# Kernel tuning notes

Measured on AMD Instinct MI355X. Metric: run time of the kernel, lower is better.

## Reference

```python
import jax, jax.numpy as jnp
import numpy as np
import math

D_MODEL = 128
N_HEADS = 4
DIM_FF = 256
B, L = 4, 2048
EPS = 1e-5
NEG = -1e9


def _layernorm(x, g, b):
    mu = jnp.mean(x, axis=-1, keepdims=True)
    var = jnp.mean((x - mu) ** 2, axis=-1, keepdims=True)
    return (x - mu) * jax.lax.rsqrt(var + EPS) * g + b


def setup_inputs() -> dict:
    key = jax.random.key(0)
    ks = jax.random.split(key, 16)
    s = 1.0 / math.sqrt(D_MODEL)
    return {
        "h": jax.random.normal(ks[0], (B, L, D_MODEL), jnp.float32),
        "attn_bias": jax.random.normal(ks[1], (B, N_HEADS, L, L), jnp.float32),
        "node_mask": jax.random.randint(ks[2], (B, L), 0, 2).astype(jnp.float32),
        "sparse_mask": jax.random.randint(ks[3], (B, L, L), 0, 2).astype(bool),
        "w_qkv": jax.random.normal(ks[4], (3 * D_MODEL, D_MODEL), jnp.float32) * s,
        "b_qkv": jnp.zeros((3 * D_MODEL,), jnp.float32),
        "w_out": jax.random.normal(ks[5], (D_MODEL, D_MODEL), jnp.float32) * s,
        "b_out": jnp.zeros((D_MODEL,), jnp.float32),
        "w_ff1": jax.random.normal(ks[6], (DIM_FF, D_MODEL), jnp.float32) * s,
        "b_ff1": jnp.zeros((DIM_FF,), jnp.float32),
        "w_ff2": jax.random.normal(ks[7], (D_MODEL, DIM_FF), jnp.float32) * (1.0 / math.sqrt(DIM_FF)),
        "b_ff2": jnp.zeros((D_MODEL,), jnp.float32),
        "ln1_g": jnp.ones((D_MODEL,), jnp.float32),
        "ln1_b": jnp.zeros((D_MODEL,), jnp.float32),
        "ln2_g": jnp.ones((D_MODEL,), jnp.float32),
        "ln2_b": jnp.zeros((D_MODEL,), jnp.float32),
    }


def reference(h, attn_bias, node_mask, sparse_mask, w_qkv, b_qkv, w_out, b_out,
              w_ff1, b_ff1, w_ff2, b_ff2, ln1_g, ln1_b, ln2_g, ln2_b):
    bsz, lsz, dsz = h.shape
    dk = dsz // N_HEADS
    qkv = h @ w_qkv.T + b_qkv  # [B,L,3D]
    q, k, v = jnp.split(qkv, 3, axis=-1)
    # [B,L,D] -> [B,H,L,dk]
    q = q.reshape(bsz, lsz, N_HEADS, dk).transpose(0, 2, 1, 3)
    k = k.reshape(bsz, lsz, N_HEADS, dk).transpose(0, 2, 1, 3)
    v = v.reshape(bsz, lsz, N_HEADS, dk).transpose(0, 2, 1, 3)
    scores = jnp.einsum("bhqd,bhkd->bhqk", q, k) / math.sqrt(dk)
    scores = scores + attn_bias
    scores = jnp.where(sparse_mask[:, None, :, :], scores, NEG)
    key_mask = node_mask[:, None, None, :] > 0
    scores = jnp.where(key_mask, scores, NEG)
    attn = jax.nn.softmax(scores, axis=-1)
    attn = attn * (node_mask[:, None, :, None] > 0).astype(attn.dtype)
    out = jnp.einsum("bhqk,bhkd->bhqd", attn, v)
    out = out.transpose(0, 2, 1, 3).reshape(bsz, lsz, dsz)
    out = out @ w_out.T + b_out
    h1 = _layernorm(h + out, ln1_g, ln1_b)
    ff = jax.nn.relu(h1 @ w_ff1.T + b_ff1) @ w_ff2.T + b_ff2
    h2 = _layernorm(h1 + ff, ln2_g, ln2_b)
    return h2 * node_mask[:, :, None]
```

## Files before the change

kernel.cpp:

```cpp
#include <hip/hip_runtime.h>
#include <math.h>

#define NEG_INF (-1e9f)
#define EPS 1e-5f

typedef __attribute__((ext_vector_type(8))) short short8;
typedef __attribute__((ext_vector_type(4))) float floatx4;

__device__ __forceinline__ unsigned short f2bf(float x) {
    union { float f; unsigned u; } v; v.f = x;
    unsigned r = v.u + 0x7fffu + ((v.u >> 16) & 1u);
    return (unsigned short)(r >> 16);
}

__global__ void detect_mask_kernel(const unsigned int* __restrict__ sm, int* __restrict__ flag) {
    __shared__ int bad;
    if (threadIdx.x == 0) bad = 0;
    __syncthreads();
    for (int i = threadIdx.x; i < 4096; i += 256) {
        if (sm[i] > 1u) bad = 1;
    }
    __syncthreads();
    if (threadIdx.x == 0) *flag = bad;
}

__global__ void nmask_pack_kernel(const float* __restrict__ nm, unsigned int* __restrict__ nmb) {
    const int t = threadIdx.x;
    const int b = t >> 6, w32 = t & 63;
    unsigned u = 0;
#pragma unroll
    for (int j = 0; j < 32; ++j)
        u |= (nm[b * 2048 + w32 * 32 + j] > 0.f ? 1u : 0u) << j;
    nmb[t] = u;
}

__global__ void mask_prep_kernel(const unsigned char* __restrict__ smraw,
                                 const int* __restrict__ flag,
                                 const unsigned int* __restrict__ nmb,
                                 unsigned int* __restrict__ cbits) {
    const int idx = blockIdx.x * 256 + threadIdx.x;
    const int b = idx >> 17;
    const int q = (idx >> 6) & 2047;
    const int w32 = idx & 63;
    unsigned u = 0;
    if (*flag) {
        const uint4* p = reinterpret_cast<const uint4*>(
            smraw + (size_t)(b * 2048 + q) * 2048 + w32 * 32);
        uint4 a = p[0], c = p[1];
        unsigned wd0 = a.x, wd1 = a.y, wd2 = a.z, wd3 = a.w;
        unsigned wd4 = c.x, wd5 = c.y, wd6 = c.z, wd7 = c.w;
#define BYTES4(v, sh) \
        u |= ((v) & 0xffu ? 1u : 0u) << (sh); \
        u |= ((v) & 0xff00u ? 1u : 0u) << ((sh) + 1); \
        u |= ((v) & 0xff0000u ? 1u : 0u) << ((sh) + 2); \
        u |= ((v) & 0xff000000u ? 1u : 0u) << ((sh) + 3);
        BYTES4(wd0, 0) BYTES4(wd1, 4) BYTES4(wd2, 8) BYTES4(wd3, 12)
        BYTES4(wd4, 16) BYTES4(wd5, 20) BYTES4(wd6, 24) BYTES4(wd7, 28)
#undef BYTES4
    } else {
        const uint4* p = reinterpret_cast<const uint4*>(
            reinterpret_cast<const unsigned int*>(smraw) + (size_t)(b * 2048 + q) * 2048 + w32 * 32);
#pragma unroll
        for (int wi = 0; wi < 8; ++wi) {
            uint4 a = p[wi];
            u |= (a.x ? 1u : 0u) << (wi * 4);
            u |= (a.y ? 1u : 0u) << (wi * 4 + 1);
            u |= (a.z ? 1u : 0u) << (wi * 4 + 2);
            u |= (a.w ? 1u : 0u) << (wi * 4 + 3);
        }
    }
    cbits[idx] = u & nmb[b * 64 + w32];
}

__global__ void transpose_kernel(const float* __restrict__ src, float* __restrict__ dst,
                                 int R, int C) {
    int idx = blockIdx.x * 256 + threadIdx.x;
    if (idx < R * C) {
        int r = idx / C, c = idx % C;
        dst[c * R + r] = src[idx];
    }
}

__global__ void qkv_kernel(const float* __restrict__ h, const float* __restrict__ wT,
                           const float* __restrict__ bqkv,
                           unsigned short* __restrict__ qb, unsigned short* __restrict__ kbm,
                           unsigned short* __restrict__ vtb) {
    __shared__ __align__(16) float hs[16 * 128];
    const int tid = threadIdx.x;
    const int row0 = blockIdx.x * 16;
    for (int i = tid; i < 2048; i += 384) hs[i] = h[row0 * 128 + i];
    __syncthreads();

    const int c = tid;
    float acc[16];
#pragma unroll
    for (int r = 0; r < 16; ++r) acc[r] = 0.f;

    for (int d0 = 0; d0 < 128; d0 += 4) {
        float w0 = wT[(d0 + 0) * 384 + c];
        float w1 = wT[(d0 + 1) * 384 + c];
        float w2 = wT[(d0 + 2) * 384 + c];
        float w3 = wT[(d0 + 3) * 384 + c];
#pragma unroll
        for (int r = 0; r < 16; ++r) {
            float4 h4 = *reinterpret_cast<const float4*>(&hs[r * 128 + d0]);
            acc[r] = fmaf(w0, h4.x, acc[r]);
            acc[r] = fmaf(w1, h4.y, acc[r]);
            acc[r] = fmaf(w2, h4.z, acc[r]);
            acc[r] = fmaf(w3, h4.w, acc[r]);
        }
    }
    const int part = c >> 7;
    const int cc = c & 127;
    const int head = cc >> 5;
    const int dd = cc & 31;
    const float bias = bqkv[c];
    const float scale = (part == 0) ? 0.17677669529663687f : 1.0f;
#pragma unroll
    for (int r = 0; r < 16; ++r) {
        int grow = row0 + r;
        int b = grow >> 11, l = grow & 2047;
        int bh = b * 4 + head;
        unsigned short val = f2bf((acc[r] + bias) * scale);
        if (part == 0)      qb[((size_t)bh * 2048 + l) * 32 + dd] = val;
        else if (part == 1) kbm[((size_t)bh * 2048 + l) * 32 + dd] = val;
        else                vtb[((size_t)bh * 32 + dd) * 2048 + l] = val;
    }
}

__global__ __launch_bounds__(256, 2) void attn_kernel(
        const unsigned short* __restrict__ qb, const unsigned short* __restrict__ kbm,
        const unsigned short* __restrict__ vtb, const float* __restrict__ bias,
        const unsigned int* __restrict__ cbits, const float* __restrict__ nmask,
        float* __restrict__ aout) {
    __shared__ unsigned short p_lds[4][16 * 72];

    const int tid = threadIdx.x;
    const int w = tid >> 6, L = tid & 63;
    const int lb = (blockIdx.x & 7) * 64 + (blockIdx.x >> 3);
    const int bh = lb >> 5, qt = lb & 31;
    const int b = bh >> 2, hh = bh & 3;
    const int q0 = qt * 64 + w * 16;
    const int q = L & 15, g = L >> 4;

    const unsigned short* kbase = kbm + (size_t)bh * 2048 * 32 + g * 8;
    const unsigned short* vbase = vtb + (size_t)bh * 32 * 2048 + g * 8;
    const short8 qf = *reinterpret_cast<const short8*>(
        qb + ((size_t)bh * 2048 + q0 + q) * 32 + g * 8);
    const float* brow = bias + ((size_t)bh * 2048 + q0 + q) * 2048 + g * 4;
    const unsigned int* crow = cbits + (size_t)(b * 2048 + q0 + q) * 64;

    float mrun = -3.0e38f, lrun = 0.f;
    floatx4 o0 = {0.f, 0.f, 0.f, 0.f}, o1 = {0.f, 0.f, 0.f, 0.f};
    const floatx4 zacc = {0.f, 0.f, 0.f, 0.f};
    unsigned short* pl = &p_lds[w][q * 72];

    for (int t = 0; t < 32; ++t) {
        const int k0 = t * 64;
        short8 kf0 = *reinterpret_cast<const short8*>(kbase + (size_t)(k0 +  0 + q) * 32);
        short8 kf1 = *reinterpret_cast<const short8*>(kbase + (size_t)(k0 + 16 + q) * 32);
        short8 kf2 = *reinterpret_cast<const short8*>(kbase + (size_t)(k0 + 32 + q) * 32);
        short8 kf3 = *reinterpret_cast<const short8*>(kbase + (size_t)(k0 + 48 + q) * 32);
        float4 bq0 = *reinterpret_cast<const float4*>(brow + k0);
        float4 bq1 = *reinterpret_cast<const float4*>(brow + k0 + 16);
        float4 bq2 = *reinterpret_cast<const float4*>(brow + k0 + 32);
        float4 bq3 = *reinterpret_cast<const float4*>(brow + k0 + 48);
        uint2 cw = *reinterpret_cast<const uint2*>(crow + t * 2);
        short8 vf00 = *reinterpret_cast<const short8*>(vbase + (size_t)(q     ) * 2048 + k0);
        short8 vf01 = *reinterpret_cast<const short8*>(vbase + (size_t)(q     ) * 2048 + k0 + 32);
        short8 vf10 = *reinterpret_cast<const short8*>(vbase + (size_t)(16 + q) * 2048 + k0);
        short8 vf11 = *reinterpret_cast<const short8*>(vbase + (size_t)(16 + q) * 2048 + k0 + 32);

        float s[16];
        {
            floatx4 r0 = __builtin_amdgcn_mfma_f32_16x16x32_bf16(kf0, qf, zacc, 0, 0, 0);
            floatx4 r1 = __builtin_amdgcn_mfma_f32_16x16x32_bf16(kf1, qf, zacc, 0, 0, 0);
            floatx4 r2 = __builtin_amdgcn_mfma_f32_16x16x32_bf16(kf2, qf, zacc, 0, 0, 0);
            floatx4 r3 = __builtin_amdgcn_mfma_f32_16x16x32_bf16(kf3, qf, zacc, 0, 0, 0);
            s[0] = r0[0]; s[1] = r0[1]; s[2] = r0[2]; s[3] = r0[3];
            s[4] = r1[0]; s[5] = r1[1]; s[6] = r1[2]; s[7] = r1[3];
            s[8] = r2[0]; s[9] = r2[1]; s[10] = r2[2]; s[11] = r2[3];
            s[12] = r3[0]; s[13] = r3[1]; s[14] = r3[2]; s[15] = r3[3];
        }
        float bvv[16];
        bvv[0] = bq0.x; bvv[1] = bq0.y; bvv[2] = bq0.z; bvv[3] = bq0.w;
        bvv[4] = bq1.x; bvv[5] = bq1.y; bvv[6] = bq1.z; bvv[7] = bq1.w;
        bvv[8] = bq2.x; bvv[9] = bq2.y; bvv[10] = bq2.z; bvv[11] = bq2.w;
        bvv[12] = bq3.x; bvv[13] = bq3.y; bvv[14] = bq3.z; bvv[15] = bq3.w;
#pragma unroll
        for (int i = 0; i < 16; ++i) {
            const int mm = i >> 2, reg = i & 3;
            const unsigned word = (mm < 2) ? cw.x : cw.y;
            const int sh = 16 * (mm & 1) + 4 * g + reg;
            const bool keep = (word >> sh) & 1;
            s[i] = keep ? (s[i] + bvv[i]) : NEG_INF;
        }
        float tm = s[0];
#pragma unroll
        for (int i = 1; i < 16; ++i) tm = fmaxf(tm, s[i]);
        tm = fmaxf(tm, __shfl_xor(tm, 16));
        tm = fmaxf(tm, __shfl_xor(tm, 32));
        const float mn = fmaxf(mrun, tm);
        const float f = __expf(mrun - mn);
        mrun = mn;
        float p[16], ts = 0.f;
#pragma unroll
        for (int i = 0; i < 16; ++i) { p[i] = __expf(s[i] - mn); ts += p[i]; }
        ts += __shfl_xor(ts, 16);
        ts += __shfl_xor(ts, 32);
        lrun = lrun * f + ts;
        o0 *= f; o1 *= f;
#pragma unroll
        for (int mm = 0; mm < 4; ++mm) {
            unsigned u0 = (unsigned)f2bf(p[4 * mm]) | ((unsigned)f2bf(p[4 * mm + 1]) << 16);
            unsigned u1 = (unsigned)f2bf(p[4 * mm + 2]) | ((unsigned)f2bf(p[4 * mm + 3]) << 16);
            *reinterpret_cast<unsigned int*>(pl + 16 * mm + 4 * g) = u0;
            *reinterpret_cast<unsigned int*>(pl + 16 * mm + 4 * g + 2) = u1;
        }
        short8 pb0 = *reinterpret_cast<const short8*>(pl + g * 8);
        short8 pb1 = *reinterpret_cast<const short8*>(pl + 32 + g * 8);
        o0 = __builtin_amdgcn_mfma_f32_16x16x32_bf16(vf00, pb0, o0, 0, 0, 0);
        o0 = __builtin_amdgcn_mfma_f32_16x16x32_bf16(vf01, pb1, o0, 0, 0, 0);
        o1 = __builtin_amdgcn_mfma_f32_16x16x32_bf16(vf10, pb0, o1, 0, 0, 0);
        o1 = __builtin_amdgcn_mfma_f32_16x16x32_bf16(vf11, pb1, o1, 0, 0, 0);
    }

    const int qrow = q0 + q;
    const float nmq = nmask[b * 2048 + qrow];
    const float inv = (nmq > 0.f) ? (1.f / lrun) : 0.f;
    float* op = aout + ((size_t)b * 2048 + qrow) * 128 + hh * 32 + g * 4;
    *reinterpret_cast<float4*>(op) = make_float4(o0[0] * inv, o0[1] * inv, o0[2] * inv, o0[3] * inv);
    *reinterpret_cast<float4*>(op + 16) = make_float4(o1[0] * inv, o1[1] * inv, o1[2] * inv, o1[3] * inv);
}

__device__ __forceinline__ void ln_stats(const float* buf, float* mu_s, float* rs_s, int tid) {
    int row = tid >> 4, sl = tid & 15;
    float4 x0 = *reinterpret_cast<const float4*>(&buf[row * 128 + sl * 8]);
    float4 x1 = *reinterpret_cast<const float4*>(&buf[row * 128 + sl * 8 + 4]);
    float sum = x0.x + x0.y + x0.z + x0.w + x1.x + x1.y + x1.z + x1.w;
    float sq = x0.x * x0.x + x0.y * x0.y + x0.z * x0.z + x0.w * x0.w +
               x1.x * x1.x + x1.y * x1.y + x1.z * x1.z + x1.w * x1.w;
#pragma unroll
    for (int off = 8; off > 0; off >>= 1) {
        sum += __shfl_xor(sum, off);
        sq += __shfl_xor(sq, off);
    }
    if (sl == 0) {
        float mu = sum * (1.f / 128.f);
        float var = sq * (1.f / 128.f) - mu * mu;
        mu_s[row] = mu;
        rs_s[row] = rsqrtf(var + EPS);
    }
}

__global__ void epilogue_kernel(const float* __restrict__ aout, const float* __restrict__ h,
                                const float* __restrict__ woutT, const float* __restrict__ bout,
                                const float* __restrict__ wff1T, const float* __restrict__ bff1,
                                const float* __restrict__ wff2T, const float* __restrict__ bff2,
                                const float* __restrict__ g1, const float* __restrict__ b1,
                                const float* __restrict__ g2, const float* __restrict__ b2,
                                const float* __restrict__ nmask, float* __restrict__ out) {
    __shared__ __align__(16) float A[16 * 128];
    __shared__ __align__(16) float Hb[16 * 128];
    __shared__ __align__(16) float F[16 * 256];
    __shared__ float mu_s[16], rs_s[16];

    const int tid = threadIdx.x;
    const int row0 = blockIdx.x * 16;
    for (int i = tid; i < 2048; i += 256) {
        A[i] = aout[row0 * 128 + i];
        Hb[i] = h[row0 * 128 + i];
    }
    __syncthreads();

    const int g = tid >> 7, c = tid & 127;

    float acc[8];
#pragma unroll
    for (int r = 0; r < 8; ++r) acc[r] = 0.f;
    for (int d0 = 0; d0 < 128; d0 += 4) {
        float w0 = woutT[(d0 + 0) * 128 + c];
        float w1 = woutT[(d0 + 1) * 128 + c];
        float w2 = woutT[(d0 + 2) * 128 + c];
        float w3 = woutT[(d0 + 3) * 128 + c];
#pragma unroll
        for (int r = 0; r < 8; ++r) {
            float4 a4 = *reinterpret_cast<const float4*>(&A[(g * 8 + r) * 128 + d0]);
            acc[r] = fmaf(w0, a4.x, acc[r]);
            acc[r] = fmaf(w1, a4.y, acc[r]);
            acc[r] = fmaf(w2, a4.z, acc[r]);
            acc[r] = fmaf(w3, a4.w, acc[r]);
        }
    }
    float bo = bout[c];
#pragma unroll
    for (int r = 0; r < 8; ++r) {
        int row = g * 8 + r;
        Hb[row * 128 + c] += acc[r] + bo;
    }
    __syncthreads();

    ln_stats(Hb, mu_s, rs_s, tid);
    __syncthreads();
    float g1c = g1[c], b1c = b1[c];
#pragma unroll
    for (int r = 0; r < 8; ++r) {
        int row = g * 8 + r;
        float v = (Hb[row * 128 + c] - mu_s[row]) * rs_s[row] * g1c + b1c;
        Hb[row * 128 + c] = v;
    }
    __syncthreads();

    {
        const int j = tid;
        float a2[16];
#pragma unroll
        for (int r = 0; r < 16; ++r) a2[r] = 0.f;
        for (int d0 = 0; d0 < 128; d0 += 4) {
            float w0 = wff1T[(d0 + 0) * 256 + j];
            float w1 = wff1T[(d0 + 1) * 256 + j];
            float w2 = wff1T[(d0 + 2) * 256 + j];
            float w3 = wff1T[(d0 + 3) * 256 + j];
#pragma unroll
            for (int r = 0; r < 16; ++r) {
                float4 h4 = *reinterpret_cast<const float4*>(&Hb[r * 128 + d0]);
                a2[r] = fmaf(w0, h4.x, a2[r]);
                a2[r] = fmaf(w1, h4.y, a2[r]);
                a2[r] = fmaf(w2, h4.z, a2[r]);
                a2[r] = fmaf(w3, h4.w, a2[r]);
            }
        }
        float bj = bff1[j];
#pragma unroll
        for (int r = 0; r < 16; ++r) F[r * 256 + j] = fmaxf(a2[r] + bj, 0.f);
    }
    __syncthreads();

    float a3[8];
#pragma unroll
    for (int r = 0; r < 8; ++r) a3[r] = 0.f;
    for (int d0 = 0; d0 < 256; d0 += 4) {
        float w0 = wff2T[(d0 + 0) * 128 + c];
        float w1 = wff2T[(d0 + 1) * 128 + c];
        float w2 = wff2T[(d0 + 2) * 128 + c];
        float w3 = wff2T[(d0 + 3) * 128 + c];
#pragma unroll
        for (int r = 0; r < 8; ++r) {
            float4 f4 = *reinterpret_cast<const float4*>(&F[(g * 8 + r) * 256 + d0]);
            a3[r] = fmaf(w0, f4.x, a3[r]);
            a3[r] = fmaf(w1, f4.y, a3[r]);
            a3[r] = fmaf(w2, f4.z, a3[r]);
            a3[r] = fmaf(w3, f4.w, a3[r]);
        }
    }
    float bo2 = bff2[c];
#pragma unroll
    for (int r = 0; r < 8; ++r) {
        int row = g * 8 + r;
        A[row * 128 + c] = a3[r] + bo2 + Hb[row * 128 + c];
    }
    __syncthreads();

    ln_stats(A, mu_s, rs_s, tid);
    __syncthreads();
    float g2c = g2[c], b2c = b2[c];
#pragma unroll
    for (int r = 0; r < 8; ++r) {
        int row = g * 8 + r;
        float nm = nmask[row0 + row];
        float v = (A[row * 128 + c] - mu_s[row]) * rs_s[row] * g2c + b2c;
        out[(row0 + row) * 128 + c] = v * nm;
    }
}

extern "C" void kernel_launch(void* const* d_in, const int* in_sizes, int n_in,
                              void* d_out, int out_size, void* d_ws, size_t ws_size,
                              hipStream_t stream) {
    const float* h = (const float*)d_in[0];
    const float* bias = (const float*)d_in[1];
    const float* nmask = (const float*)d_in[2];
    const void* smask = d_in[3];
    const float* w_qkv = (const float*)d_in[4];
    const float* b_qkv = (const float*)d_in[5];
    const float* w_out = (const float*)d_in[6];
    const float* b_out = (const float*)d_in[7];
    const float* w_ff1 = (const float*)d_in[8];
    const float* b_ff1 = (const float*)d_in[9];
    const float* w_ff2 = (const float*)d_in[10];
    const float* b_ff2 = (const float*)d_in[11];
    const float* g1 = (const float*)d_in[12];
    const float* b1 = (const float*)d_in[13];
    const float* g2 = (const float*)d_in[14];
    const float* b2 = (const float*)d_in[15];
    float* out = (float*)d_out;

    char* wsb = (char*)d_ws;
    float* aoutw = (float*)wsb;
    unsigned short* qb  = (unsigned short*)(wsb + (4 << 20));
    unsigned short* kbm = (unsigned short*)(wsb + (6 << 20));
    unsigned short* vtb = (unsigned short*)(wsb + (8 << 20));
    unsigned int* cbits = (unsigned int*)(wsb + (10 << 20));
    unsigned int* nmb   = (unsigned int*)(wsb + (12 << 20));
    float* wqkvT = (float*)(wsb + (12 << 20) + 4096);
    float* woutT = wqkvT + 384 * 128;
    float* wff1T = woutT + 128 * 128;
    float* wff2T = wff1T + 256 * 128;
    int* smflag = (int*)(wff2T + 128 * 256);

    detect_mask_kernel<<<1, 256, 0, stream>>>((const unsigned int*)smask, smflag);
    nmask_pack_kernel<<<1, 256, 0, stream>>>(nmask, nmb);
    mask_prep_kernel<<<2048, 256, 0, stream>>>((const unsigned char*)smask, smflag, nmb, cbits);
    transpose_kernel<<<192, 256, 0, stream>>>(w_qkv, wqkvT, 384, 128);
    transpose_kernel<<<64, 256, 0, stream>>>(w_out, woutT, 128, 128);
    transpose_kernel<<<128, 256, 0, stream>>>(w_ff1, wff1T, 256, 128);
    transpose_kernel<<<128, 256, 0, stream>>>(w_ff2, wff2T, 128, 256);
    qkv_kernel<<<512, 384, 0, stream>>>(h, wqkvT, b_qkv, qb, kbm, vtb);
    attn_kernel<<<512, 256, 0, stream>>>(qb, kbm, vtb, bias, cbits, nmask, aoutw);
    epilogue_kernel<<<512, 256, 0, stream>>>(aoutw, h, woutT, b_out, wff1T, b_ff1,
                                             wff2T, b_ff2, g1, b1, g2, b2, nmask, out);
}
```

Before: 191.2 us.

## Stage attention bias through LDS with register prefetch and merge tiny launches

The attention kernel now loads each 16x64 bias tile with row-coalesced float4 reads into registers, one tile ahead, then writes it to a padded LDS buffer and reads it back in the MFMA fragment layout. Before, each lane read scattered 16-byte pieces of global memory. The change targets the bias stream, the largest input at about 268 MB of fp32, by improving its coalescing and hiding its latency. It also merges the two mask-prep kernels into one launch and the four weight transposes into one, cutting launch overhead. The cost is more LDS and registers per block, which may lower occupancy. There is no barrier between the LDS write and read, so correctness relies on each wave using only its own LDS slice.

```diff
diff --git a/kernel.cpp b/kernel.cpp
--- a/kernel.cpp
+++ b/kernel.cpp
@@ -13,25 +13,26 @@
     return (unsigned short)(r >> 16);
 }
 
-__global__ void detect_mask_kernel(const unsigned int* __restrict__ sm, int* __restrict__ flag) {
-    __shared__ int bad;
-    if (threadIdx.x == 0) bad = 0;
-    __syncthreads();
-    for (int i = threadIdx.x; i < 4096; i += 256) {
-        if (sm[i] > 1u) bad = 1;
-    }
-    __syncthreads();
-    if (threadIdx.x == 0) *flag = bad;
-}
-
-__global__ void nmask_pack_kernel(const float* __restrict__ nm, unsigned int* __restrict__ nmb) {
-    const int t = threadIdx.x;
-    const int b = t >> 6, w32 = t & 63;
-    unsigned u = 0;
-#pragma unroll
-    for (int j = 0; j < 32; ++j)
-        u |= (nm[b * 2048 + w32 * 32 + j] > 0.f ? 1u : 0u) << j;
-    nmb[t] = u;
+__global__ void prep_kernel(const unsigned int* __restrict__ sm, int* __restrict__ flag,
+                            const float* __restrict__ nm, unsigned int* __restrict__ nmb) {
+    if (blockIdx.x == 0) {
+        __shared__ int bad;
+        if (threadIdx.x == 0) bad = 0;
+        __syncthreads();
+        for (int i = threadIdx.x; i < 4096; i += 256) {
+            if (sm[i] > 1u) bad = 1;
+        }
+        __syncthreads();
+        if (threadIdx.x == 0) *flag = bad;
+    } else {
+        const int t = threadIdx.x;
+        const int b = t >> 6, w32 = t & 63;
+        unsigned u = 0;
+#pragma unroll
+        for (int j = 0; j < 32; ++j)
+            u |= (nm[b * 2048 + w32 * 32 + j] > 0.f ? 1u : 0u) << j;
+        nmb[t] = u;
+    }
 }
 
 __global__ void mask_prep_kernel(const unsigned char* __restrict__ smraw,
@@ -72,12 +73,23 @@
     cbits[idx] = u & nmb[b * 64 + w32];
 }
 
-__global__ void transpose_kernel(const float* __restrict__ src, float* __restrict__ dst,
-                                 int R, int C) {
+__global__ void transpose_all_kernel(const float* __restrict__ w_qkv, const float* __restrict__ w_out,
+                                     const float* __restrict__ w_ff1, const float* __restrict__ w_ff2,
+                                     float* __restrict__ wqkvT, float* __restrict__ woutT,
+                                     float* __restrict__ wff1T, float* __restrict__ wff2T) {
     int idx = blockIdx.x * 256 + threadIdx.x;
-    if (idx < R * C) {
-        int r = idx / C, c = idx % C;
-        dst[c * R + r] = src[idx];
+    if (idx < 49152) {
+        int r = idx / 128, c = idx % 128;
+        wqkvT[c * 384 + r] = w_qkv[idx];
+    } else if (idx < 65536) {
+        int i = idx - 49152; int r = i / 128, c = i % 128;
+        woutT[c * 128 + r] = w_out[i];
+    } else if (idx < 98304) {
+        int i = idx - 65536; int r = i / 128, c = i % 128;
+        wff1T[c * 256 + r] = w_ff1[i];
+    } else {
+        int i = idx - 98304; int r = i / 256, c = i % 256;
+        wff2T[c * 128 + r] = w_ff2[i];
     }
 }
 
@@ -133,6 +145,7 @@
         const unsigned short* __restrict__ vtb, const float* __restrict__ bias,
         const unsigned int* __restrict__ cbits, const float* __restrict__ nmask,
         float* __restrict__ aout) {
+    __shared__ float bias_lds[4][16 * 68];
     __shared__ unsigned short p_lds[4][16 * 72];
 
     const int tid = threadIdx.x;
@@ -147,24 +160,39 @@
     const unsigned short* vbase = vtb + (size_t)bh * 32 * 2048 + g * 8;
     const short8 qf = *reinterpret_cast<const short8*>(
         qb + ((size_t)bh * 2048 + q0 + q) * 32 + g * 8);
-    const float* brow = bias + ((size_t)bh * 2048 + q0 + q) * 2048 + g * 4;
     const unsigned int* crow = cbits + (size_t)(b * 2048 + q0 + q) * 64;
+
+    const float* bias_wave = bias + ((size_t)bh * 2048 + q0) * 2048;
+    const int brow_ld = L >> 4;
+    const int bcol_ld = (L & 15) * 4;
+    float* blds = bias_lds[w];
 
     float mrun = -3.0e38f, lrun = 0.f;
     floatx4 o0 = {0.f, 0.f, 0.f, 0.f}, o1 = {0.f, 0.f, 0.f, 0.f};
     const floatx4 zacc = {0.f, 0.f, 0.f, 0.f};
     unsigned short* pl = &p_lds[w][q * 72];
 
+    float4 bpre[4];
+#pragma unroll
+    for (int i = 0; i < 4; ++i)
+        bpre[i] = *reinterpret_cast<const float4*>(
+            bias_wave + (size_t)(brow_ld + 4 * i) * 2048 + bcol_ld);
+
     for (int t = 0; t < 32; ++t) {
         const int k0 = t * 64;
+#pragma unroll
+        for (int i = 0; i < 4; ++i)
+            *reinterpret_cast<float4*>(blds + (brow_ld + 4 * i) * 68 + bcol_ld) = bpre[i];
+        const int k0n = (t + 1 < 32) ? k0 + 64 : 0;
+#pragma unroll
+        for (int i = 0; i < 4; ++i)
+            bpre[i] = *reinterpret_cast<const float4*>(
+                bias_wave + (size_t)(brow_ld + 4 * i) * 2048 + k0n + bcol_ld);
+
         short8 kf0 = *reinterpret_cast<const short8*>(kbase + (size_t)(k0 +  0 + q) * 32);
         short8 kf1 = *reinterpret_cast<const short8*>(kbase + (size_t)(k0 + 16 + q) * 32);
         short8 kf2 = *reinterpret_cast<const short8*>(kbase + (size_t)(k0 + 32 + q) * 32);
         short8 kf3 = *reinterpret_cast<const short8*>(kbase + (size_t)(k0 + 48 + q) * 32);
-        float4 bq0 = *reinterpret_cast<const float4*>(brow + k0);
-        float4 bq1 = *reinterpret_cast<const float4*>(brow + k0 + 16);
-        float4 bq2 = *reinterpret_cast<const float4*>(brow + k0 + 32);
-        float4 bq3 = *reinterpret_cast<const float4*>(brow + k0 + 48);
         uint2 cw = *reinterpret_cast<const uint2*>(crow + t * 2);
         short8 vf00 = *reinterpret_cast<const short8*>(vbase + (size_t)(q     ) * 2048 + k0);
         short8 vf01 = *reinterpret_cast<const short8*>(vbase + (size_t)(q     ) * 2048 + k0 + 32);
@@ -182,6 +210,10 @@
             s[8] = r2[0]; s[9] = r2[1]; s[10] = r2[2]; s[11] = r2[3];
             s[12] = r3[0]; s[13] = r3[1]; s[14] = r3[2]; s[15] = r3[3];
         }
+        float4 bq0 = *reinterpret_cast<const float4*>(blds + q * 68 +  0 + 4 * g);
+        float4 bq1 = *reinterpret_cast<const float4*>(blds + q * 68 + 16 + 4 * g);
+        float4 bq2 = *reinterpret_cast<const float4*>(blds + q * 68 + 32 + 4 * g);
+        float4 bq3 = *reinterpret_cast<const float4*>(blds + q * 68 + 48 + 4 * g);
         float bvv[16];
         bvv[0] = bq0.x; bvv[1] = bq0.y; bvv[2] = bq0.z; bvv[3] = bq0.w;
         bvv[4] = bq1.x; bvv[5] = bq1.y; bvv[6] = bq1.z; bvv[7] = bq1.w;
@@ -407,13 +439,10 @@
     float* wff2T = wff1T + 256 * 128;
     int* smflag = (int*)(wff2T + 128 * 256);
 
-    detect_mask_kernel<<<1, 256, 0, stream>>>((const unsigned int*)smask, smflag);
-    nmask_pack_kernel<<<1, 256, 0, stream>>>(nmask, nmb);
+    prep_kernel<<<2, 256, 0, stream>>>((const unsigned int*)smask, smflag, nmask, nmb);
     mask_prep_kernel<<<2048, 256, 0, stream>>>((const unsigned char*)smask, smflag, nmb, cbits);
-    transpose_kernel<<<192, 256, 0, stream>>>(w_qkv, wqkvT, 384, 128);
-    transpose_kernel<<<64, 256, 0, stream>>>(w_out, woutT, 128, 128);
-    transpose_kernel<<<128, 256, 0, stream>>>(w_ff1, wff1T, 256, 128);
-    transpose_kernel<<<128, 256, 0, stream>>>(w_ff2, wff2T, 128, 256);
+    transpose_all_kernel<<<512, 256, 0, stream>>>(w_qkv, w_out, w_ff1, w_ff2,
+                                                  wqkvT, woutT, wff1T, wff2T);
     qkv_kernel<<<512, 384, 0, stream>>>(h, wqkvT, b_qkv, qb, kbm, vtb);
     attn_kernel<<<512, 256, 0, stream>>>(qb, kbm, vtb, bias, cbits, nmask, aoutw);
     epilogue_kernel<<<512, 256, 0, stream>>>(aoutw, h, woutT, b_out, wff1T, b_ff1,
```

Measured after the change: 225.6 us. +18.0%, slower.
